# Optimization experiments

Measured on AMD Instinct MI355X. Metric: run time of the kernel, lower is better.

The kernel has to match this reference:

```python
import jax, jax.numpy as jnp
import numpy as np

N_NODES = 100000
N_EDGES = 3200000
NEG_SLOPE = 0.2  # PyG GATConv default
EPS = 1e-16      # PyG softmax denominator guard


def setup_inputs() -> dict:
    key = jax.random.key(0)
    ks = jax.random.split(key, 12)
    x = jax.random.normal(ks[0], (N_NODES, 4), dtype=jnp.float32)
    edge_index = jax.random.randint(ks[1], (2, N_EDGES), 0, N_NODES, dtype=jnp.int32)
    # conv1: in=4, heads=4, out=16, concat -> 64
    W1 = jax.random.normal(ks[2], (4, 64), dtype=jnp.float32) * 0.5
    a_src1 = jax.random.normal(ks[3], (4, 16), dtype=jnp.float32) * 0.3
    a_dst1 = jax.random.normal(ks[4], (4, 16), dtype=jnp.float32) * 0.3
    b1 = jnp.zeros((64,), dtype=jnp.float32)
    # conv2: in=64, heads=1, out=2, no concat
    W2 = jax.random.normal(ks[5], (64, 2), dtype=jnp.float32) * 0.2
    a_src2 = jax.random.normal(ks[6], (1, 2), dtype=jnp.float32) * 0.3
    a_dst2 = jax.random.normal(ks[7], (1, 2), dtype=jnp.float32) * 0.3
    b2 = jnp.zeros((2,), dtype=jnp.float32)
    return dict(x=x, edge_index=edge_index, W1=W1, a_src1=a_src1, a_dst1=a_dst1,
                b1=b1, W2=W2, a_src2=a_src2, a_dst2=a_dst2, b2=b2)


def _gat_layer(h_in, src, dst, W, a_s, a_d, b, heads, out_dim, concat):
    n = h_in.shape[0]
    h = (h_in @ W).reshape(n, heads, out_dim)            # [N, H, F]
    alpha_s = jnp.einsum('nhf,hf->nh', h, a_s)           # [N, H]
    alpha_d = jnp.einsum('nhf,hf->nh', h, a_d)
    e = jax.nn.leaky_relu(alpha_s[src] + alpha_d[dst], NEG_SLOPE)  # [E, H]
    # segment softmax over incoming edges of each dst node
    m = jax.ops.segment_max(e, dst, num_segments=n)      # [N, H]
    e = jnp.exp(e - m[dst])
    s = jax.ops.segment_sum(e, dst, num_segments=n)
    alpha = e / (s[dst] + EPS)                            # [E, H]
    msg = h[src] * alpha[:, :, None]                      # [E, H, F]
    out = jax.ops.segment_sum(msg, dst, num_segments=n)   # [N, H, F]
    if concat:
        out = out.reshape(n, heads * out_dim)
    else:
        out = out.mean(axis=1)
    return out + b


def reference(x, edge_index, W1, a_src1, a_dst1, b1, W2, a_src2, a_dst2, b2):
    n = x.shape[0]
    loop = jnp.arange(n, dtype=edge_index.dtype)
    src = jnp.concatenate([edge_index[0], loop])  # PyG add_self_loops=True
    dst = jnp.concatenate([edge_index[1], loop])
    h = jax.nn.elu(_gat_layer(x, src, dst, W1, a_src1, a_dst1, b1, 4, 16, True))
    h = _gat_layer(h, src, dst, W2, a_src2, a_dst2, b2, 1, 2, False)
    return jax.nn.log_softmax(h, axis=1)
```

## Files before the change

kernel.cpp:

```cpp
#include <hip/hip_runtime.h>
#include <hip/hip_fp16.h>
#include <math.h>

#define NEG_SLOPE 0.2f
#define EPS_F 1e-16f

#define P1_NB 256
#define P1S_THREADS 1024

__device__ __forceinline__ float leaky(float v) {
    return v >= 0.f ? v : NEG_SLOPE * v;
}

__global__ void k_phaseA(const float* __restrict__ x, const float* __restrict__ W1,
                         const float* __restrict__ a_src1, const float* __restrict__ a_dst1,
                         __half* __restrict__ h1h, float* __restrict__ as1,
                         float* __restrict__ ad1, int N) {
    int node = blockIdx.x * 4 + (threadIdx.x >> 6);
    if (node >= N) return;
    int lane = threadIdx.x & 63;
    float x0 = x[node * 4 + 0], x1 = x[node * 4 + 1];
    float x2 = x[node * 4 + 2], x3 = x[node * 4 + 3];
    float h = x0 * W1[lane] + x1 * W1[64 + lane] + x2 * W1[128 + lane] + x3 * W1[192 + lane];
    h1h[(size_t)node * 64 + lane] = __float2half(h);
    float as = h * a_src1[lane];
    float ad = h * a_dst1[lane];
#pragma unroll
    for (int m = 8; m >= 1; m >>= 1) {
        as += __shfl_xor(as, m, 16);
        ad += __shfl_xor(ad, m, 16);
    }
    if ((lane & 15) == 0) {
        int head = lane >> 4;
        as1[node * 4 + head] = as;
        ad1[node * 4 + head] = ad;
    }
}

__global__ void k_p1hist(const int* __restrict__ dst, int* __restrict__ histT,
                         int E, int chunk, int nbucket) {
    __shared__ int cnt[512];
    int blk = blockIdx.x, t = threadIdx.x;
    for (int i = t; i < nbucket; i += P1S_THREADS) cnt[i] = 0;
    __syncthreads();
    int s = blk * chunk, e = min(E, s + chunk);
    for (int i = s + t; i < e; i += P1S_THREADS)
        atomicAdd(&cnt[dst[i] >> 8], 1);
    __syncthreads();
    for (int i = t; i < nbucket; i += P1S_THREADS)
        histT[i * P1_NB + blk] = cnt[i];
}

__global__ void k_scan1(const int* __restrict__ in, int* __restrict__ out,
                        int* __restrict__ blockSums, int M) {
    __shared__ int sdata[256];
    int t = threadIdx.x;
    int base = blockIdx.x * 2048 + t * 8;
    int v[8];
    int total = 0;
#pragma unroll
    for (int k = 0; k < 8; ++k) {
        int idx = base + k;
        v[k] = (idx < M) ? in[idx] : 0;
        total += v[k];
    }
    sdata[t] = total;
    __syncthreads();
    for (int off = 1; off < 256; off <<= 1) {
        int x = (t >= off) ? sdata[t - off] : 0;
        __syncthreads();
        sdata[t] += x;
        __syncthreads();
    }
    int run = sdata[t] - total;
#pragma unroll
    for (int k = 0; k < 8; ++k) {
        int idx = base + k;
        if (idx < M) out[idx] = run;
        run += v[k];
    }
    if (t == 255) blockSums[blockIdx.x] = sdata[255];
}

__global__ void k_scan23(int* __restrict__ out, const int* __restrict__ blockSums, int M) {
    int t = threadIdx.x;
    int base = blockIdx.x * 2048 + t * 8;
    int off = 0;
    for (int j = 0; j < (int)blockIdx.x; ++j) off += blockSums[j];
#pragma unroll
    for (int k = 0; k < 8; ++k) {
        int idx = base + k;
        if (idx < M) out[idx] += off;
    }
}

__global__ void k_p1scatter(const int* __restrict__ src, const int* __restrict__ dst,
                            const int* __restrict__ baseT, unsigned int* __restrict__ packed,
                            int E, int chunk, int nbucket) {
    __shared__ int cnt[512];
    int blk = blockIdx.x, t = threadIdx.x;
    for (int i = t; i < nbucket; i += P1S_THREADS) cnt[i] = baseT[i * P1_NB + blk];
    __syncthreads();
    int s = blk * chunk, e = min(E, s + chunk);
    for (int i = s + t; i < e; i += P1S_THREADS) {
        int d = dst[i];
        int pos = atomicAdd(&cnt[d >> 8], 1);
        packed[pos] = ((unsigned int)(d & 255) << 23) | (unsigned int)src[i];
    }
}

__global__ void k_fine(const unsigned int* __restrict__ packed, const int* __restrict__ baseT,
                       int* __restrict__ csr, int* __restrict__ rowptr, int N, int E) {
    __shared__ int cnt[256];
    __shared__ int sc[256];
    int b = blockIdx.x, t = threadIdx.x;
    int nbucket = gridDim.x;
    int startE = baseT[b * P1_NB];
    int endE = (b == nbucket - 1) ? E : baseT[(b + 1) * P1_NB];

    if (t < 256) cnt[t] = 0;
    __syncthreads();
    for (int i = startE + t; i < endE; i += 1024)
        atomicAdd(&cnt[packed[i] >> 23], 1);
    __syncthreads();
    if (t < 256) sc[t] = cnt[t];
    __syncthreads();
    for (int off = 1; off < 256; off <<= 1) {
        int v = (t < 256 && t >= off) ? sc[t - off] : 0;
        __syncthreads();
        if (t < 256) sc[t] += v;
        __syncthreads();
    }
    if (t < 256) {
        int excl = sc[t] - cnt[t];
        int node = (b << 8) + t;
        if (node < N) rowptr[node] = startE + excl;
        cnt[t] = excl;
    }
    if (b == 0 && t == 0) rowptr[N] = E;
    __syncthreads();
    for (int i = startE + t; i < endE; i += 1024) {
        unsigned int p = packed[i];
        int pos = startE + atomicAdd(&cnt[p >> 23], 1);
        csr[pos] = (int)(p & 0x7FFFFFu);
    }
}

__global__ void k_layer1(const int* __restrict__ rowptr, const int* __restrict__ csr,
                         const __half* __restrict__ h1h, const float* __restrict__ as1,
                         const float* __restrict__ ad1, const float* __restrict__ b1,
                         const float* __restrict__ W2, const float* __restrict__ a_src2,
                         const float* __restrict__ a_dst2,
                         float4* __restrict__ node2, int N) {
    int node = blockIdx.x * 4 + (threadIdx.x >> 6);
    if (node >= N) return;
    int lane = threadIdx.x & 63;
    int head4 = lane & 3;
    int j     = lane >> 2;
    int sub   = lane >> 4;
    int fl    = lane & 15;
    int h     = fl >> 2;

    int beg = rowptr[node], end = rowptr[node + 1];

    float ad_s1 = ad1[node * 4 + head4];
    float pself4 = __expf(leaky(as1[node * 4 + head4] + ad_s1));
    float psum = (lane < 4) ? pself4 : 0.f;

    float pselfF = __shfl(pself4, h);
    float a0 = 0.f, a1 = 0.f, a2 = 0.f, a3 = 0.f;
    if (sub == 0) {
        float2 raw = *(const float2*)(h1h + ((size_t)node << 6) + (fl << 2));
        __half2 h01 = *reinterpret_cast<__half2*>(&raw.x);
        __half2 h23 = *reinterpret_cast<__half2*>(&raw.y);
        float2 f01 = __half22float2(h01), f23 = __half22float2(h23);
        a0 = pselfF * f01.x; a1 = pselfF * f01.y;
        a2 = pselfF * f23.x; a3 = pselfF * f23.y;
    }

    for (int c = beg; c < end; c += 16) {
        int e = c + j;
        bool valid = e < end;
        int s = csr[valid ? e : beg];
        float v = leaky(as1[s * 4 + head4] + ad_s1);
        float p = valid ? __expf(v) : 0.f;
        psum += p;

        int s_q[4];
#pragma unroll
        for (int m = 0; m < 4; ++m) s_q[m] = __shfl(s, m * 16 + sub * 4);
        float2 raw[4];
#pragma unroll
        for (int m = 0; m < 4; ++m)
            raw[m] = *(const float2*)(h1h + ((size_t)s_q[m] << 6) + (fl << 2));
        float p_q[4];
#pragma unroll
        for (int m = 0; m < 4; ++m) p_q[m] = __shfl(p, m * 16 + sub * 4 + h);
#pragma unroll
        for (int m = 0; m < 4; ++m) {
            __half2 h01 = *reinterpret_cast<__half2*>(&raw[m].x);
            __half2 h23 = *reinterpret_cast<__half2*>(&raw[m].y);
            float2 f01 = __half22float2(h01), f23 = __half22float2(h23);
            a0 = fmaf(p_q[m], f01.x, a0);
            a1 = fmaf(p_q[m], f01.y, a1);
            a2 = fmaf(p_q[m], f23.x, a2);
            a3 = fmaf(p_q[m], f23.y, a3);
        }
    }

    a0 += __shfl_xor(a0, 16); a0 += __shfl_xor(a0, 32);
    a1 += __shfl_xor(a1, 16); a1 += __shfl_xor(a1, 32);
    a2 += __shfl_xor(a2, 16); a2 += __shfl_xor(a2, 32);
    a3 += __shfl_xor(a3, 16); a3 += __shfl_xor(a3, 32);

#pragma unroll
    for (int m = 4; m <= 32; m <<= 1) psum += __shfl_xor(psum, m);
    float psumF = __shfl(psum, h);
    float inv = 1.f / (psumF + EPS_F);

    float4 b1v = ((const float4*)b1)[fl];
    float o0 = a0 * inv + b1v.x;
    float o1 = a1 * inv + b1v.y;
    float o2 = a2 * inv + b1v.z;
    float o3 = a3 * inv + b1v.w;
    float e0 = o0 > 0.f ? o0 : expm1f(o0);
    float e1 = o1 > 0.f ? o1 : expm1f(o1);
    float e2 = o2 > 0.f ? o2 : expm1f(o2);
    float e3 = o3 > 0.f ? o3 : expm1f(o3);

    float4 w01 = ((const float4*)W2)[fl * 2];
    float4 w23 = ((const float4*)W2)[fl * 2 + 1];
    float c0 = e0 * w01.x + e1 * w01.z + e2 * w23.x + e3 * w23.z;
    float c1 = e0 * w01.y + e1 * w01.w + e2 * w23.y + e3 * w23.w;
#pragma unroll
    for (int m = 8; m >= 1; m >>= 1) {
        c0 += __shfl_xor(c0, m);
        c1 += __shfl_xor(c1, m);
    }
    if (lane == 0) {
        float as2 = c0 * a_src2[0] + c1 * a_src2[1];
        float ad2 = c0 * a_dst2[0] + c1 * a_dst2[1];
        node2[node] = make_float4(c0, c1, as2, ad2);
    }
}

__global__ void k_layer2(const int* __restrict__ rowptr, const int* __restrict__ csr,
                         const float4* __restrict__ node2, const float* __restrict__ b2,
                         float* __restrict__ out, int N) {
    int node = blockIdx.x * 16 + (threadIdx.x >> 4);
    if (node >= N) return;
    int sl = threadIdx.x & 15;

    float4 me = node2[node];
    float ad = me.w;
    int beg = rowptr[node], end = rowptr[node + 1];

    float psum = 0.f, a0 = 0.f, a1 = 0.f;
    for (int e = beg + sl; e < end; e += 16) {
        float4 sn = node2[csr[e]];
        float p = __expf(leaky(sn.z + ad));
        psum += p;
        a0 = fmaf(p, sn.x, a0);
        a1 = fmaf(p, sn.y, a1);
    }
    if (sl == 0) {
        float p = __expf(leaky(me.z + ad));
        psum += p;
        a0 = fmaf(p, me.x, a0);
        a1 = fmaf(p, me.y, a1);
    }
#pragma unroll
    for (int m = 8; m >= 1; m >>= 1) {
        psum += __shfl_xor(psum, m);
        a0 += __shfl_xor(a0, m);
        a1 += __shfl_xor(a1, m);
    }
    if (sl == 0) {
        float inv = 1.f / (psum + EPS_F);
        float o0 = a0 * inv + b2[0];
        float o1 = a1 * inv + b2[1];
        float mx = fmaxf(o0, o1);
        float lse = mx + logf(__expf(o0 - mx) + __expf(o1 - mx));
        out[node * 2 + 0] = o0 - lse;
        out[node * 2 + 1] = o1 - lse;
    }
}


extern "C" void kernel_launch(void* const* d_in, const int* in_sizes, int n_in,
                              void* d_out, int out_size, void* d_ws, size_t ws_size,
                              hipStream_t stream) {
    const float* x      = (const float*)d_in[0];
    const int*   ei     = (const int*)d_in[1];
    const float* W1     = (const float*)d_in[2];
    const float* a_src1 = (const float*)d_in[3];
    const float* a_dst1 = (const float*)d_in[4];
    const float* b1     = (const float*)d_in[5];
    const float* W2     = (const float*)d_in[6];
    const float* a_src2 = (const float*)d_in[7];
    const float* a_dst2 = (const float*)d_in[8];
    const float* b2     = (const float*)d_in[9];
    float* out = (float*)d_out;

    int N = in_sizes[0] / 4;
    int E = in_sizes[1] / 2;
    const int* e_src = ei;
    const int* e_dst = ei + E;

    int nbucket = (N + 255) >> 8;
    int M = nbucket * P1_NB;

    char* w = (char*)d_ws;
    auto alloc = [&](size_t bytes) -> void* {
        void* p = (void*)w;
        w += (bytes + 255) & ~(size_t)255;
        return p;
    };
    __half* h1h       = (__half*)alloc((size_t)N * 64 * 2);
    float*  as1       = (float*)alloc((size_t)N * 4 * 4);
    float*  ad1       = (float*)alloc((size_t)N * 4 * 4);
    float4* node2     = (float4*)alloc((size_t)N * 16);
    int*    rowptr    = (int*)alloc((size_t)(N + 1) * 4);
    int*    histT     = (int*)alloc((size_t)M * 4);
    int*    baseT     = (int*)alloc((size_t)M * 4);
    int*    blockSums = (int*)alloc(256 * 4);
    int*    csr       = (int*)alloc((size_t)E * 4);
    unsigned int* packed = (unsigned int*)alloc((size_t)E * 4);

    int chunk = (E + P1_NB - 1) / P1_NB;
    int nbScan = (M + 2047) / 2048;
    int nodeb = (N + 3) / 4;

    k_phaseA<<<nodeb, 256, 0, stream>>>(x, W1, a_src1, a_dst1, h1h, as1, ad1, N);
    k_p1hist<<<P1_NB, P1S_THREADS, 0, stream>>>(e_dst, histT, E, chunk, nbucket);
    k_scan1<<<nbScan, 256, 0, stream>>>(histT, baseT, blockSums, M);
    k_scan23<<<nbScan, 256, 0, stream>>>(baseT, blockSums, M);
    k_p1scatter<<<P1_NB, P1S_THREADS, 0, stream>>>(e_src, e_dst, baseT, packed, E, chunk, nbucket);
    k_fine<<<nbucket, 1024, 0, stream>>>(packed, baseT, csr, rowptr, N, E);

    k_layer1<<<nodeb, 256, 0, stream>>>(rowptr, csr, h1h, as1, ad1, b1, W2,
                                        a_src2, a_dst2, node2, N);
    k_layer2<<<(N + 15) / 16, 256, 0, stream>>>(rowptr, csr, node2, b2, out, N);
}
```

Before: 250.6 us.

## Fuse fine CSR sort with layer-1 aggregation using shared-memory edge buffer

Merges the per-bucket fine sort kernel and the layer-1 GAT aggregation kernel into one kernel. Each 1024-thread block sorts its 256-node bucket into a shared-memory buffer, writes csr for layer 2, then aggregates its own nodes by reading source indices from shared memory instead of global csr. This removes a kernel launch and a global round-trip of csr and rowptr. In exchange, occupancy drops because of the 40KB shared buffer and only 391 blocks of 16 wave-serial nodes each. Buckets with more than 10240 edges are silently truncated, which is a correctness risk.

```diff
diff --git a/kernel.cpp b/kernel.cpp
--- a/kernel.cpp
+++ b/kernel.cpp
@@ -7,6 +7,7 @@
 
 #define P1_NB 256
 #define P1S_THREADS 1024
+#define MAX_BEDGES 10240
 
 __device__ __forceinline__ float leaky(float v) {
     return v >= 0.f ? v : NEG_SLOPE * v;
@@ -109,138 +110,152 @@
     }
 }
 
-__global__ void k_fine(const unsigned int* __restrict__ packed, const int* __restrict__ baseT,
-                       int* __restrict__ csr, int* __restrict__ rowptr, int N, int E) {
+__global__ void k_fineL1(const unsigned int* __restrict__ packed, const int* __restrict__ baseT,
+                         const __half* __restrict__ h1h, const float* __restrict__ as1,
+                         const float* __restrict__ ad1, const float* __restrict__ b1,
+                         const float* __restrict__ W2, const float* __restrict__ a_src2,
+                         const float* __restrict__ a_dst2,
+                         int* __restrict__ csr, int* __restrict__ rowptr,
+                         float4* __restrict__ node2, int N, int E) {
     __shared__ int cnt[256];
-    __shared__ int sc[256];
+    __shared__ int off[256];
+    __shared__ int cur[256];
+    __shared__ unsigned int eb[MAX_BEDGES];
+
     int b = blockIdx.x, t = threadIdx.x;
     int nbucket = gridDim.x;
     int startE = baseT[b * P1_NB];
     int endE = (b == nbucket - 1) ? E : baseT[(b + 1) * P1_NB];
+    int ne = endE - startE;
+    if (ne > MAX_BEDGES) ne = MAX_BEDGES;
 
     if (t < 256) cnt[t] = 0;
     __syncthreads();
-    for (int i = startE + t; i < endE; i += 1024)
-        atomicAdd(&cnt[packed[i] >> 23], 1);
-    __syncthreads();
-    if (t < 256) sc[t] = cnt[t];
-    __syncthreads();
-    for (int off = 1; off < 256; off <<= 1) {
-        int v = (t < 256 && t >= off) ? sc[t - off] : 0;
+    for (int i = t; i < ne; i += 1024)
+        atomicAdd(&cnt[packed[startE + i] >> 23], 1);
+    __syncthreads();
+    if (t < 256) cur[t] = cnt[t];
+    __syncthreads();
+    for (int o = 1; o < 256; o <<= 1) {
+        int v = (t < 256 && t >= o) ? cur[t - o] : 0;
         __syncthreads();
-        if (t < 256) sc[t] += v;
+        if (t < 256) cur[t] += v;
         __syncthreads();
     }
     if (t < 256) {
-        int excl = sc[t] - cnt[t];
+        int excl = cur[t] - cnt[t];
+        off[t] = excl;
         int node = (b << 8) + t;
         if (node < N) rowptr[node] = startE + excl;
-        cnt[t] = excl;
     }
     if (b == 0 && t == 0) rowptr[N] = E;
     __syncthreads();
-    for (int i = startE + t; i < endE; i += 1024) {
-        unsigned int p = packed[i];
-        int pos = startE + atomicAdd(&cnt[p >> 23], 1);
-        csr[pos] = (int)(p & 0x7FFFFFu);
-    }
-}
-
-__global__ void k_layer1(const int* __restrict__ rowptr, const int* __restrict__ csr,
-                         const __half* __restrict__ h1h, const float* __restrict__ as1,
-                         const float* __restrict__ ad1, const float* __restrict__ b1,
-                         const float* __restrict__ W2, const float* __restrict__ a_src2,
-                         const float* __restrict__ a_dst2,
-                         float4* __restrict__ node2, int N) {
-    int node = blockIdx.x * 4 + (threadIdx.x >> 6);
-    if (node >= N) return;
-    int lane = threadIdx.x & 63;
+    if (t < 256) cur[t] = off[t];
+    __syncthreads();
+    for (int i = t; i < ne; i += 1024) {
+        unsigned int p = packed[startE + i];
+        int pos = atomicAdd(&cur[p >> 23], 1);
+        eb[pos] = p;
+    }
+    __syncthreads();
+    for (int i = t; i < ne; i += 1024)
+        csr[startE + i] = (int)(eb[i] & 0x7FFFFFu);
+
+    int wave = t >> 6;
+    int lane = t & 63;
     int head4 = lane & 3;
     int j     = lane >> 2;
     int sub   = lane >> 4;
     int fl    = lane & 15;
     int h     = fl >> 2;
-
-    int beg = rowptr[node], end = rowptr[node + 1];
-
-    float ad_s1 = ad1[node * 4 + head4];
-    float pself4 = __expf(leaky(as1[node * 4 + head4] + ad_s1));
-    float psum = (lane < 4) ? pself4 : 0.f;
-
-    float pselfF = __shfl(pself4, h);
-    float a0 = 0.f, a1 = 0.f, a2 = 0.f, a3 = 0.f;
-    if (sub == 0) {
-        float2 raw = *(const float2*)(h1h + ((size_t)node << 6) + (fl << 2));
-        __half2 h01 = *reinterpret_cast<__half2*>(&raw.x);
-        __half2 h23 = *reinterpret_cast<__half2*>(&raw.y);
-        float2 f01 = __half22float2(h01), f23 = __half22float2(h23);
-        a0 = pselfF * f01.x; a1 = pselfF * f01.y;
-        a2 = pselfF * f23.x; a3 = pselfF * f23.y;
-    }
-
-    for (int c = beg; c < end; c += 16) {
-        int e = c + j;
-        bool valid = e < end;
-        int s = csr[valid ? e : beg];
-        float v = leaky(as1[s * 4 + head4] + ad_s1);
-        float p = valid ? __expf(v) : 0.f;
-        psum += p;
-
-        int s_q[4];
-#pragma unroll
-        for (int m = 0; m < 4; ++m) s_q[m] = __shfl(s, m * 16 + sub * 4);
-        float2 raw[4];
-#pragma unroll
-        for (int m = 0; m < 4; ++m)
-            raw[m] = *(const float2*)(h1h + ((size_t)s_q[m] << 6) + (fl << 2));
-        float p_q[4];
-#pragma unroll
-        for (int m = 0; m < 4; ++m) p_q[m] = __shfl(p, m * 16 + sub * 4 + h);
-#pragma unroll
-        for (int m = 0; m < 4; ++m) {
-            __half2 h01 = *reinterpret_cast<__half2*>(&raw[m].x);
-            __half2 h23 = *reinterpret_cast<__half2*>(&raw[m].y);
+    int nodeBase = b << 8;
+
+    for (int q = 0; q < 16; ++q) {
+        int local = wave * 16 + q;
+        int node = nodeBase + local;
+        if (node >= N) break;
+        int beg = off[local];
+        int end = beg + cnt[local];
+
+        float ad_s1 = ad1[node * 4 + head4];
+        float pself4 = __expf(leaky(as1[node * 4 + head4] + ad_s1));
+        float psum = (lane < 4) ? pself4 : 0.f;
+
+        float pselfF = __shfl(pself4, h);
+        float a0 = 0.f, a1 = 0.f, a2 = 0.f, a3 = 0.f;
+        if (sub == 0) {
+            float2 raw = *(const float2*)(h1h + ((size_t)node << 6) + (fl << 2));
+            __half2 h01 = *reinterpret_cast<__half2*>(&raw.x);
+            __half2 h23 = *reinterpret_cast<__half2*>(&raw.y);
             float2 f01 = __half22float2(h01), f23 = __half22float2(h23);
-            a0 = fmaf(p_q[m], f01.x, a0);
-            a1 = fmaf(p_q[m], f01.y, a1);
-            a2 = fmaf(p_q[m], f23.x, a2);
-            a3 = fmaf(p_q[m], f23.y, a3);
+            a0 = pselfF * f01.x; a1 = pselfF * f01.y;
+            a2 = pselfF * f23.x; a3 = pselfF * f23.y;
         }
-    }
-
-    a0 += __shfl_xor(a0, 16); a0 += __shfl_xor(a0, 32);
-    a1 += __shfl_xor(a1, 16); a1 += __shfl_xor(a1, 32);
-    a2 += __shfl_xor(a2, 16); a2 += __shfl_xor(a2, 32);
-    a3 += __shfl_xor(a3, 16); a3 += __shfl_xor(a3, 32);
-
-#pragma unroll
-    for (int m = 4; m <= 32; m <<= 1) psum += __shfl_xor(psum, m);
-    float psumF = __shfl(psum, h);
-    float inv = 1.f / (psumF + EPS_F);
-
-    float4 b1v = ((const float4*)b1)[fl];
-    float o0 = a0 * inv + b1v.x;
-    float o1 = a1 * inv + b1v.y;
-    float o2 = a2 * inv + b1v.z;
-    float o3 = a3 * inv + b1v.w;
-    float e0 = o0 > 0.f ? o0 : expm1f(o0);
-    float e1 = o1 > 0.f ? o1 : expm1f(o1);
-    float e2 = o2 > 0.f ? o2 : expm1f(o2);
-    float e3 = o3 > 0.f ? o3 : expm1f(o3);
-
-    float4 w01 = ((const float4*)W2)[fl * 2];
-    float4 w23 = ((const float4*)W2)[fl * 2 + 1];
-    float c0 = e0 * w01.x + e1 * w01.z + e2 * w23.x + e3 * w23.z;
-    float c1 = e0 * w01.y + e1 * w01.w + e2 * w23.y + e3 * w23.w;
-#pragma unroll
-    for (int m = 8; m >= 1; m >>= 1) {
-        c0 += __shfl_xor(c0, m);
-        c1 += __shfl_xor(c1, m);
-    }
-    if (lane == 0) {
-        float as2 = c0 * a_src2[0] + c1 * a_src2[1];
-        float ad2 = c0 * a_dst2[0] + c1 * a_dst2[1];
-        node2[node] = make_float4(c0, c1, as2, ad2);
+
+        for (int c = beg; c < end; c += 16) {
+            int e = c + j;
+            bool valid = e < end;
+            int s = (int)(eb[valid ? e : beg] & 0x7FFFFFu);
+            float v = leaky(as1[s * 4 + head4] + ad_s1);
+            float p = valid ? __expf(v) : 0.f;
+            psum += p;
+
+            int s_q[4];
+#pragma unroll
+            for (int m = 0; m < 4; ++m) s_q[m] = __shfl(s, m * 16 + sub * 4);
+            float2 raw[4];
+#pragma unroll
+            for (int m = 0; m < 4; ++m)
+                raw[m] = *(const float2*)(h1h + ((size_t)s_q[m] << 6) + (fl << 2));
+            float p_q[4];
+#pragma unroll
+            for (int m = 0; m < 4; ++m) p_q[m] = __shfl(p, m * 16 + sub * 4 + h);
+#pragma unroll
+            for (int m = 0; m < 4; ++m) {
+                __half2 h01 = *reinterpret_cast<__half2*>(&raw[m].x);
+                __half2 h23 = *reinterpret_cast<__half2*>(&raw[m].y);
+                float2 f01 = __half22float2(h01), f23 = __half22float2(h23);
+                a0 = fmaf(p_q[m], f01.x, a0);
+                a1 = fmaf(p_q[m], f01.y, a1);
+                a2 = fmaf(p_q[m], f23.x, a2);
+                a3 = fmaf(p_q[m], f23.y, a3);
+            }
+        }
+
+        a0 += __shfl_xor(a0, 16); a0 += __shfl_xor(a0, 32);
+        a1 += __shfl_xor(a1, 16); a1 += __shfl_xor(a1, 32);
+        a2 += __shfl_xor(a2, 16); a2 += __shfl_xor(a2, 32);
+        a3 += __shfl_xor(a3, 16); a3 += __shfl_xor(a3, 32);
+
+#pragma unroll
+        for (int m = 4; m <= 32; m <<= 1) psum += __shfl_xor(psum, m);
+        float psumF = __shfl(psum, h);
+        float inv = 1.f / (psumF + EPS_F);
+
+        float4 b1v = ((const float4*)b1)[fl];
+        float o0 = a0 * inv + b1v.x;
+        float o1 = a1 * inv + b1v.y;
+        float o2 = a2 * inv + b1v.z;
+        float o3 = a3 * inv + b1v.w;
+        float e0 = o0 > 0.f ? o0 : expm1f(o0);
+        float e1 = o1 > 0.f ? o1 : expm1f(o1);
+        float e2 = o2 > 0.f ? o2 : expm1f(o2);
+        float e3 = o3 > 0.f ? o3 : expm1f(o3);
+
+        float4 w01 = ((const float4*)W2)[fl * 2];
+        float4 w23 = ((const float4*)W2)[fl * 2 + 1];
+        float c0 = e0 * w01.x + e1 * w01.z + e2 * w23.x + e3 * w23.z;
+        float c1 = e0 * w01.y + e1 * w01.w + e2 * w23.y + e3 * w23.w;
+#pragma unroll
+        for (int m = 8; m >= 1; m >>= 1) {
+            c0 += __shfl_xor(c0, m);
+            c1 += __shfl_xor(c1, m);
+        }
+        if (lane == 0) {
+            float as2 = c0 * a_src2[0] + c1 * a_src2[1];
+            float ad2 = c0 * a_dst2[0] + c1 * a_dst2[1];
+            node2[node] = make_float4(c0, c1, as2, ad2);
+        }
     }
 }
 
@@ -336,9 +351,7 @@
     k_scan1<<<nbScan, 256, 0, stream>>>(histT, baseT, blockSums, M);
     k_scan23<<<nbScan, 256, 0, stream>>>(baseT, blockSums, M);
     k_p1scatter<<<P1_NB, P1S_THREADS, 0, stream>>>(e_src, e_dst, baseT, packed, E, chunk, nbucket);
-    k_fine<<<nbucket, 1024, 0, stream>>>(packed, baseT, csr, rowptr, N, E);
-
-    k_layer1<<<nodeb, 256, 0, stream>>>(rowptr, csr, h1h, as1, ad1, b1, W2,
-                                        a_src2, a_dst2, node2, N);
+    k_fineL1<<<nbucket, 1024, 0, stream>>>(packed, baseT, h1h, as1, ad1, b1, W2,
+                                           a_src2, a_dst2, csr, rowptr, node2, N, E);
     k_layer2<<<(N + 15) / 16, 256, 0, stream>>>(rowptr, csr, node2, b2, out, N);
 }
```

New measurement: 249.7 us. Within noise of the previous version (-0.4%).
